# Performance work log

Hardware: AMD Instinct MI355X
Metric: run time of the kernel (lower is better)

The kernel has to match this reference:

```python
import jax, jax.numpy as jnp
import numpy as np

NUM_HEADS = 16
ROPE_BASE = 10000.0

def _rope(x):
    # x: (B, T, H, hd), rotate-half 1D RoPE over temporal axis
    B, T, H, hd = x.shape
    inv_freq = 1.0 / (ROPE_BASE ** (jnp.arange(0, hd, 2, dtype=jnp.float32) / hd))  # (hd/2,)
    freqs = jnp.arange(T, dtype=jnp.float32)[:, None] * inv_freq[None, :]            # (T, hd/2)
    emb = jnp.concatenate([freqs, freqs], axis=-1)                                    # (T, hd)
    cos = jnp.cos(emb)[None, :, None, :]
    sin = jnp.sin(emb)[None, :, None, :]
    x1, x2 = jnp.split(x, 2, axis=-1)
    rot = jnp.concatenate([-x2, x1], axis=-1)
    return x * cos + rot * sin

def setup_inputs() -> dict:
    key = jax.random.key(0)
    ks = jax.random.split(key, 7)
    B, T, S, D = 4, 16, 256, 2048
    std = 0.02
    return {
        'v_p': jax.random.normal(ks[0], (B, T, S, D), jnp.float32),
        'v_f': jax.random.normal(ks[1], (B, T, S, D), jnp.float32),
        'a_p': jax.random.normal(ks[2], (B, T, D), jnp.float32),
        'a_f': jax.random.normal(ks[3], (B, T, D), jnp.float32),
        'W_qkv': jax.random.normal(ks[4], (D, 3 * D), jnp.float32) * std,
        'W_proj': jax.random.normal(ks[5], (D, D), jnp.float32) * std,
        'b_proj': jnp.zeros((D,), jnp.float32),
    }

def reference(v_p, v_f, a_p, a_f, W_qkv, W_proj, b_proj):
    B, T_p, S, D = v_p.shape
    T_f = v_f.shape[1]
    H = NUM_HEADS
    hd = D // H
    scale = hd ** -0.5
    # pool spatial dim and concatenate streams: [v_p, v_f, a_p, a_f]
    tokens = jnp.concatenate([v_p.mean(axis=2), v_f.mean(axis=2), a_p, a_f], axis=1)  # (B, T, D)
    T = tokens.shape[1]
    qkv = tokens @ W_qkv  # qkv_bias=False
    q, k, v = jnp.split(qkv, 3, axis=-1)
    q = q.reshape(B, T, H, hd)
    k = k.reshape(B, T, H, hd)
    v = v.reshape(B, T, H, hd)
    q = _rope(q)
    k = _rope(k)
    scores = jnp.einsum('bqhd,bkhd->bhqk', q, k) * scale
    causal_mask = jnp.triu(jnp.ones((T, T), dtype=bool), k=1)
    scores = jnp.where(causal_mask[None, None], -jnp.inf, scores)
    attn = jax.nn.softmax(scores, axis=-1)
    out = jnp.einsum('bhqk,bkhd->bqhd', attn, v).reshape(B, T, D)
    out = out @ W_proj + b_proj
    v_p_out = jnp.broadcast_to(out[:, :T_p, None, :], (B, T_p, S, D))
    v_f_out = jnp.broadcast_to(out[:, T_p:T_p + T_f, None, :], (B, T_f, S, D))
    a_p_out = out[:, T_p + T_f:T_p + T_f + T_p]
    a_f_out = out[:, T_p + T_f + T_p:]
    return (v_p_out, v_f_out, a_p_out, a_f_out)
```

## Files before the change

kernel.cpp:

```cpp
#include <hip/hip_runtime.h>
#include <hip/hip_bf16.h>
#include <stdint.h>


using bf16x8v = __attribute__((ext_vector_type(8))) __bf16;
using f32x4v  = __attribute__((ext_vector_type(4))) float;

union Pack8 { __bf16 h[8]; uint4 u; };
union Pack4 { __bf16 h[4]; uint2 u; };

__device__ __forceinline__ int swz(int r, int c) {
    return (r << 6) + ((c ^ (r & 7)) << 3);
}
__device__ __forceinline__ int aswz(int r, int c) {
    return (r << 7) + ((c ^ (r & 31)) << 2);
}

__global__ __launch_bounds__(256) void prep_mean_kernel(
    const float* __restrict__ v_p, const float* __restrict__ v_f,
    float* __restrict__ partials,
    const float* __restrict__ W_qkv, const float* __restrict__ W_proj,
    __bf16* __restrict__ Wt_qkv, __bf16* __restrict__ Wt_proj)
{
    __shared__ float Ls[64][68];
    int bid0 = blockIdx.x;
    if (bid0 < 2048) {
        int bid = bid0;
        int which  = bid >> 10;
        int rem    = bid & 1023;
        int row    = rem >> 4;
        int dchunk = (rem >> 3) & 1;
        int schunk = rem & 7;
        int d = (dchunk << 10) + (threadIdx.x << 2);
        const float* src = (which ? v_f : v_p) + ((size_t)row << 19)
                         + ((size_t)(schunk << 5) << 11) + d;
        float4 a = {0.f, 0.f, 0.f, 0.f};
        #pragma unroll 16
        for (int s = 0; s < 32; ++s) {
            float4 x = *reinterpret_cast<const float4*>(src + ((size_t)s << 11));
            a.x += x.x; a.y += x.y; a.z += x.z; a.w += x.w;
        }
        int pr = which * 64 + row;
        *reinterpret_cast<float4*>(&partials[(size_t)((pr << 3) + schunk) * 2048 + d]) = a;
    } else {
        int bid = bid0 - 2048;
        const float* src; __bf16* dst; int N, tile;
        if (bid < 3072) { src = W_qkv;  dst = Wt_qkv;  N = 6144; tile = bid; }
        else            { src = W_proj; dst = Wt_proj; N = 2048; tile = bid - 3072; }
        int tiles_n = N >> 6;
        int tn = tile % tiles_n;
        int tk = tile / tiles_n;
        int t = threadIdx.x;
        int rb = t >> 4;
        int c4 = (t & 15) << 2;
        #pragma unroll
        for (int s = 0; s < 4; ++s) {
            int r = rb + (s << 4);
            float4 v = *reinterpret_cast<const float4*>(
                src + (size_t)(tk * 64 + r) * N + tn * 64 + c4);
            *reinterpret_cast<float4*>(&Ls[r][c4]) = v;
        }
        __syncthreads();
        int c  = t >> 2;
        int r0 = (t & 3) << 4;
        Pack8 p0, p1;
        #pragma unroll
        for (int i = 0; i < 8; ++i) p0.h[i] = (__bf16)Ls[r0 + i][c];
        #pragma unroll
        for (int i = 0; i < 8; ++i) p1.h[i] = (__bf16)Ls[r0 + 8 + i][c];
        __bf16* drow = dst + (size_t)(tn * 64 + c) * 2048 + tk * 64 + r0;
        *reinterpret_cast<uint4*>(drow)     = p0.u;
        *reinterpret_cast<uint4*>(drow + 8) = p1.u;
    }
}

__global__ __launch_bounds__(256) void tokens_finish_kernel(
    const float* __restrict__ partials, const float* __restrict__ a_p,
    const float* __restrict__ a_f, __bf16* __restrict__ tokens_bf)
{
    int bid = blockIdx.x;
    if (bid < 128) {
        int idx = (bid * 256 + threadIdx.x) * 8;
        int r = idx >> 11;
        int d = idx & 2047;
        float s[8];
        #pragma unroll
        for (int i = 0; i < 8; ++i) s[i] = 0.f;
        #pragma unroll
        for (int sc = 0; sc < 8; ++sc) {
            const float* p = partials + (size_t)((r << 3) + sc) * 2048 + d;
            float4 x0 = *reinterpret_cast<const float4*>(p);
            float4 x1 = *reinterpret_cast<const float4*>(p + 4);
            s[0] += x0.x; s[1] += x0.y; s[2] += x0.z; s[3] += x0.w;
            s[4] += x1.x; s[5] += x1.y; s[6] += x1.z; s[7] += x1.w;
        }
        const float inv = 1.f / 256.f;
        int which = r >> 6, rr = r & 63;
        int b = rr >> 4, tt = rr & 15;
        int tokrow = b * 64 + which * 16 + tt;
        Pack8 p;
        #pragma unroll
        for (int i = 0; i < 8; ++i) p.h[i] = (__bf16)(s[i] * inv);
        *reinterpret_cast<uint4*>(&tokens_bf[(size_t)tokrow * 2048 + d]) = p.u;
    } else {
        int g = (bid - 128) * 256 + threadIdx.x;
        int which = g >> 14;
        int j = g & 16383;
        int b = j >> 12;
        int rr = j & 4095;
        int tt = rr >> 8;
        int gq = rr & 255;
        const float* src = (which ? a_f : a_p) + (size_t)(b * 16 + tt) * 2048 + gq * 8;
        float4 x0 = *reinterpret_cast<const float4*>(src);
        float4 x1 = *reinterpret_cast<const float4*>(src + 4);
        Pack8 p;
        p.h[0] = (__bf16)x0.x; p.h[1] = (__bf16)x0.y; p.h[2] = (__bf16)x0.z; p.h[3] = (__bf16)x0.w;
        p.h[4] = (__bf16)x1.x; p.h[5] = (__bf16)x1.y; p.h[6] = (__bf16)x1.z; p.h[7] = (__bf16)x1.w;
        int tokrow = b * 64 + 32 + which * 16 + tt;
        *reinterpret_cast<uint4*>(&tokens_bf[(size_t)tokrow * 2048 + gq * 8]) = p.u;
    }
}

__global__ __launch_bounds__(256) void gemm_bf16_kernel(
    const __bf16* __restrict__ A, const __bf16* __restrict__ Bt,
    float* __restrict__ C, int N)
{
    __shared__ __bf16 As[4096];
    __shared__ __bf16 Bs[4096];
    const int t = threadIdx.x;
    const int m0 = blockIdx.y << 6;
    const int n0 = blockIdx.x << 6;
    const int kz = blockIdx.z;
    const int kbase = kz << 10;
    const int lane = t & 63;
    const int w = t >> 6;
    const int wm = w << 4;
    const int lrow = lane & 15;
    const int lk = lane >> 4;
    const int srl = lane >> 3;
    const int schunk = lane & 7;

    f32x4v acc[4] = {{0.f,0.f,0.f,0.f},{0.f,0.f,0.f,0.f},
                     {0.f,0.f,0.f,0.f},{0.f,0.f,0.f,0.f}};

    int row_c0 = (w << 4) + srl;
    int row_c1 = row_c0 + 8;
    const __bf16* gA0 = A  + (size_t)(m0 + row_c0) * 2048 + kbase + ((schunk ^ (row_c0 & 7)) << 3);
    const __bf16* gA1 = A  + (size_t)(m0 + row_c1) * 2048 + kbase + ((schunk ^ (row_c1 & 7)) << 3);
    const __bf16* gB0 = Bt + (size_t)(n0 + row_c0) * 2048 + kbase + ((schunk ^ (row_c0 & 7)) << 3);
    const __bf16* gB1 = Bt + (size_t)(n0 + row_c1) * 2048 + kbase + ((schunk ^ (row_c1 & 7)) << 3);
    __bf16* lA0 = &As[(w << 4) << 6];
    __bf16* lA1 = &As[((w << 4) + 8) << 6];
    __bf16* lB0 = &Bs[(w << 4) << 6];
    __bf16* lB1 = &Bs[((w << 4) + 8) << 6];

    for (int kt = 0; kt < 16; ++kt) {
        __syncthreads();
        int ko = kt << 6;
        __builtin_amdgcn_global_load_lds(
            (const __attribute__((address_space(1))) void*)(gA0 + ko),
            (__attribute__((address_space(3))) void*)lA0, 16, 0, 0);
        __builtin_amdgcn_global_load_lds(
            (const __attribute__((address_space(1))) void*)(gA1 + ko),
            (__attribute__((address_space(3))) void*)lA1, 16, 0, 0);
        __builtin_amdgcn_global_load_lds(
            (const __attribute__((address_space(1))) void*)(gB0 + ko),
            (__attribute__((address_space(3))) void*)lB0, 16, 0, 0);
        __builtin_amdgcn_global_load_lds(
            (const __attribute__((address_space(1))) void*)(gB1 + ko),
            (__attribute__((address_space(3))) void*)lB1, 16, 0, 0);
        __syncthreads();
        #pragma unroll
        for (int s = 0; s < 2; ++s) {
            int cA = (s << 2) + lk;
            bf16x8v af = *reinterpret_cast<const bf16x8v*>(&As[swz(wm + lrow, cA)]);
            #pragma unroll
            for (int j = 0; j < 4; ++j) {
                bf16x8v bf = *reinterpret_cast<const bf16x8v*>(&Bs[swz((j << 4) + lrow, cA)]);
                acc[j] = __builtin_amdgcn_mfma_f32_16x16x32_bf16(af, bf, acc[j], 0, 0, 0);
            }
        }
    }
    float* Cz = C + (size_t)kz * 256 * N;
    #pragma unroll
    for (int j = 0; j < 4; ++j) {
        int col = n0 + (j << 4) + lrow;
        #pragma unroll
        for (int e = 0; e < 4; ++e) {
            int row = m0 + wm + (lk << 2) + e;
            Cz[(size_t)row * N + col] = acc[j][e];
        }
    }
}

__global__ __launch_bounds__(256) void attn_kernel(
    const float* __restrict__ qkv, __bf16* __restrict__ attn_out)
{
    __shared__ float q_s[16 * 128];
    __shared__ float k_s[64 * 128];
    const size_t PART = (size_t)256 * 6144;
    int bid = blockIdx.x;
    int qt = bid & 3;
    int h  = (bid >> 2) & 15;
    int b  = bid >> 6;
    int tid = threadIdx.x;
    int qr0 = qt << 4;
    int kcap = qr0 + 16;
    const float* base0 = qkv + (size_t)(b * 64) * 6144 + h * 128;
    const float* base1 = base0 + PART;
    const float L2C = 0.20762050593046012f;
    const float scale = 0.0883883476483184405f;

    {
        int tq = tid >> 4;
        int cg = tid & 15;
        int d = cg << 2;
        int grow = qr0 + tq;
        const float* s0 = base0 + (size_t)grow * 6144;
        const float* s1 = base1 + (size_t)grow * 6144;
        float4 q1a = *reinterpret_cast<const float4*>(s0 + d);
        float4 q1b = *reinterpret_cast<const float4*>(s1 + d);
        float4 q2a = *reinterpret_cast<const float4*>(s0 + d + 64);
        float4 q2b = *reinterpret_cast<const float4*>(s1 + d + 64);
        float4 q1 = {q1a.x + q1b.x, q1a.y + q1b.y, q1a.z + q1b.z, q1a.w + q1b.w};
        float4 q2 = {q2a.x + q2b.x, q2a.y + q2b.y, q2a.z + q2b.z, q2a.w + q2b.w};
        float ft = (float)grow;
        float a0 = ft * exp2f(-(float)(d + 0) * L2C);
        float a1 = ft * exp2f(-(float)(d + 1) * L2C);
        float a2 = ft * exp2f(-(float)(d + 2) * L2C);
        float a3 = ft * exp2f(-(float)(d + 3) * L2C);
        float c0 = cosf(a0), s0f = sinf(a0);
        float c1 = cosf(a1), s1f = sinf(a1);
        float c2 = cosf(a2), s2f = sinf(a2);
        float c3 = cosf(a3), s3f = sinf(a3);
        float4 qa, qb;
        qa.x = q1.x * c0 - q2.x * s0f;  qb.x = q2.x * c0 + q1.x * s0f;
        qa.y = q1.y * c1 - q2.y * s1f;  qb.y = q2.y * c1 + q1.y * s1f;
        qa.z = q1.z * c2 - q2.z * s2f;  qb.z = q2.z * c2 + q1.z * s2f;
        qa.w = q1.w * c3 - q2.w * s3f;  qb.w = q2.w * c3 + q1.w * s3f;
        *reinterpret_cast<float4*>(&q_s[aswz(tq, cg)])      = qa;
        *reinterpret_cast<float4*>(&q_s[aswz(tq, cg + 16)]) = qb;
    }
    #pragma unroll
    for (int r = 0; r < 4; ++r) {
        int idx = tid + (r << 8);
        if (idx < (kcap << 4)) {
            int tk = idx >> 4;
            int cg = idx & 15;
            int d = cg << 2;
            const float* s0 = base0 + (size_t)tk * 6144 + 2048;
            const float* s1 = base1 + (size_t)tk * 6144 + 2048;
            float4 k1a = *reinterpret_cast<const float4*>(s0 + d);
            float4 k1b = *reinterpret_cast<const float4*>(s1 + d);
            float4 k2a = *reinterpret_cast<const float4*>(s0 + d + 64);
            float4 k2b = *reinterpret_cast<const float4*>(s1 + d + 64);
            float4 k1 = {k1a.x + k1b.x, k1a.y + k1b.y, k1a.z + k1b.z, k1a.w + k1b.w};
            float4 k2 = {k2a.x + k2b.x, k2a.y + k2b.y, k2a.z + k2b.z, k2a.w + k2b.w};
            float ft = (float)tk;
            float a0 = ft * exp2f(-(float)(d + 0) * L2C);
            float a1 = ft * exp2f(-(float)(d + 1) * L2C);
            float a2 = ft * exp2f(-(float)(d + 2) * L2C);
            float a3 = ft * exp2f(-(float)(d + 3) * L2C);
            float c0 = cosf(a0), s0f = sinf(a0);
            float c1 = cosf(a1), s1f = sinf(a1);
            float c2 = cosf(a2), s2f = sinf(a2);
            float c3 = cosf(a3), s3f = sinf(a3);
            float4 ka, kb;
            ka.x = k1.x * c0 - k2.x * s0f;  kb.x = k2.x * c0 + k1.x * s0f;
            ka.y = k1.y * c1 - k2.y * s1f;  kb.y = k2.y * c1 + k1.y * s1f;
            ka.z = k1.z * c2 - k2.z * s2f;  kb.z = k2.z * c2 + k1.z * s2f;
            ka.w = k1.w * c3 - k2.w * s3f;  kb.w = k2.w * c3 + k1.w * s3f;
            *reinterpret_cast<float4*>(&k_s[aswz(tk, cg)])      = ka;
            *reinterpret_cast<float4*>(&k_s[aswz(tk, cg + 16)]) = kb;
        }
    }
    __syncthreads();
    int qi = tid >> 4;
    int g  = tid & 15;
    int qg = qr0 + qi;
    float pv[4] = {0.f, 0.f, 0.f, 0.f};
    for (int c = 0; c < 32; ++c) {
        float4 a = *reinterpret_cast<const float4*>(&q_s[aswz(qi, c)]);
        #pragma unroll
        for (int j = 0; j < 4; ++j) {
            if ((j << 4) < kcap) {
                int ki = (j << 4) + g;
                float4 bb = *reinterpret_cast<const float4*>(&k_s[aswz(ki, c)]);
                pv[j] += a.x * bb.x + a.y * bb.y + a.z * bb.z + a.w * bb.w;
            }
        }
    }
    float m = -1e30f;
    #pragma unroll
    for (int j = 0; j < 4; ++j) {
        if ((j << 4) < kcap) {
            int ki = (j << 4) + g;
            pv[j] = (ki <= qg) ? pv[j] * scale : -1e30f;
            m = fmaxf(m, pv[j]);
        }
    }
    m = fmaxf(m, __shfl_xor(m, 1));
    m = fmaxf(m, __shfl_xor(m, 2));
    m = fmaxf(m, __shfl_xor(m, 4));
    m = fmaxf(m, __shfl_xor(m, 8));
    float l = 0.f;
    #pragma unroll
    for (int j = 0; j < 4; ++j) {
        if ((j << 4) < kcap) {
            float e = (pv[j] > -1e29f) ? expf(pv[j] - m) : 0.f;
            pv[j] = e;
            l += e;
        }
    }
    l += __shfl_xor(l, 1);
    l += __shfl_xor(l, 2);
    l += __shfl_xor(l, 4);
    l += __shfl_xor(l, 8);
    float inv_l = 1.f / l;
    __syncthreads();
    float* p_s = q_s;
    #pragma unroll
    for (int j = 0; j < 4; ++j) {
        if ((j << 4) < kcap) p_s[qi * 65 + (j << 4) + g] = pv[j] * inv_l;
    }
    float* v_s = k_s;
    #pragma unroll
    for (int r = 0; r < 8; ++r) {
        int idx = tid + (r << 8);
        if (idx < (kcap << 5)) {
            int tv = idx >> 5;
            int c = idx & 31;
            float4 va = *reinterpret_cast<const float4*>(base0 + (size_t)tv * 6144 + 4096 + (c << 2));
            float4 vb = *reinterpret_cast<const float4*>(base1 + (size_t)tv * 6144 + 4096 + (c << 2));
            float4 vs = {va.x + vb.x, va.y + vb.y, va.z + vb.z, va.w + vb.w};
            *reinterpret_cast<float4*>(&v_s[aswz(tv, c)]) = vs;
        }
    }
    __syncthreads();
    float4 acc[2] = {{0.f,0.f,0.f,0.f},{0.f,0.f,0.f,0.f}};
    for (int ki = 0; ki < kcap; ++ki) {
        float p = p_s[qi * 65 + ki];
        #pragma unroll
        for (int u = 0; u < 2; ++u) {
            float4 vv = *reinterpret_cast<const float4*>(&v_s[aswz(ki, (g << 1) + u)]);
            acc[u].x += p * vv.x;
            acc[u].y += p * vv.y;
            acc[u].z += p * vv.z;
            acc[u].w += p * vv.w;
        }
    }
    __bf16* orow = attn_out + (size_t)(b * 64 + qg) * 2048 + h * 128 + (g << 3);
    #pragma unroll
    for (int u = 0; u < 2; ++u) {
        Pack4 p4;
        p4.h[0] = (__bf16)acc[u].x; p4.h[1] = (__bf16)acc[u].y;
        p4.h[2] = (__bf16)acc[u].z; p4.h[3] = (__bf16)acc[u].w;
        *reinterpret_cast<uint2*>(orow + (u << 2)) = p4.u;
    }
}

__global__ __launch_bounds__(256) void outputs_kernel(
    const float* __restrict__ outp, const float* __restrict__ b_proj,
    float* __restrict__ d_out)
{
    const size_t PART = (size_t)256 * 2048;
    int bid = blockIdx.x;
    if (bid < 4096) {
        int which = bid >> 11;
        int rem = bid & 2047;
        int row = rem >> 5;
        int schunk = rem & 31;
        int b = row >> 4;
        int t = row & 15;
        size_t srcoff = (size_t)(b * 64 + (which << 4) + t) * 2048 + threadIdx.x * 8;
        const float* s0 = outp + srcoff;
        const float* s1 = outp + PART + srcoff;
        float4 a0 = *reinterpret_cast<const float4*>(s0);
        float4 a1 = *reinterpret_cast<const float4*>(s0 + 4);
        float4 b0 = *reinterpret_cast<const float4*>(s1);
        float4 b1 = *reinterpret_cast<const float4*>(s1 + 4);
        float4 v0 = *reinterpret_cast<const float4*>(b_proj + threadIdx.x * 8);
        float4 v1 = *reinterpret_cast<const float4*>(b_proj + threadIdx.x * 8 + 4);
        float4 o0 = {a0.x + b0.x + v0.x, a0.y + b0.y + v0.y,
                     a0.z + b0.z + v0.z, a0.w + b0.w + v0.w};
        float4 o1 = {a1.x + b1.x + v1.x, a1.y + b1.y + v1.y,
                     a1.z + b1.z + v1.z, a1.w + b1.w + v1.w};
        size_t base = (size_t)which * 33554432 +
                      ((size_t)row * 256 + (size_t)schunk * 8) * 2048 + threadIdx.x * 8;
        float* dst = d_out + base;
        #pragma unroll
        for (int s = 0; s < 8; ++s) {
            *reinterpret_cast<float4*>(dst + (size_t)s * 2048)     = o0;
            *reinterpret_cast<float4*>(dst + (size_t)s * 2048 + 4) = o1;
        }
    } else {
        int g8 = (bid - 4096) * 256 + threadIdx.x;
        int which = g8 >> 14;
        int j = g8 & 16383;
        int b = j >> 12;
        int rr = j & 4095;
        int tt = rr >> 8;
        int gq = rr & 255;
        size_t srcoff = (size_t)(b * 64 + 32 + (which << 4) + tt) * 2048 + gq * 8;
        const float* s0 = outp + srcoff;
        const float* s1 = outp + PART + srcoff;
        float4 a0 = *reinterpret_cast<const float4*>(s0);
        float4 a1 = *reinterpret_cast<const float4*>(s0 + 4);
        float4 b0 = *reinterpret_cast<const float4*>(s1);
        float4 b1 = *reinterpret_cast<const float4*>(s1 + 4);
        float4 v0 = *reinterpret_cast<const float4*>(b_proj + gq * 8);
        float4 v1 = *reinterpret_cast<const float4*>(b_proj + gq * 8 + 4);
        float4 x0 = {a0.x + b0.x + v0.x, a0.y + b0.y + v0.y,
                     a0.z + b0.z + v0.z, a0.w + b0.w + v0.w};
        float4 x1 = {a1.x + b1.x + v1.x, a1.y + b1.y + v1.y,
                     a1.z + b1.z + v1.z, a1.w + b1.w + v1.w};
        float* dst = d_out + 67108864 + (size_t)which * 131072 +
                     (size_t)(b * 16 + tt) * 2048 + gq * 8;
        *reinterpret_cast<float4*>(dst)     = x0;
        *reinterpret_cast<float4*>(dst + 4) = x1;
    }
}

extern "C" void kernel_launch(void* const* d_in, const int* in_sizes, int n_in,
                              void* d_out, int out_size, void* d_ws, size_t ws_size,
                              hipStream_t stream)
{
    const float* v_p    = (const float*)d_in[0];
    const float* v_f    = (const float*)d_in[1];
    const float* a_p    = (const float*)d_in[2];
    const float* a_f    = (const float*)d_in[3];
    const float* W_qkv  = (const float*)d_in[4];
    const float* W_proj = (const float*)d_in[5];
    const float* b_proj = (const float*)d_in[6];
    float* out_f = (float*)d_out;

    char* ws = (char*)d_ws;
    __bf16* tokens_bf = (__bf16*)(ws);
    __bf16* Wt_qkv    = (__bf16*)(ws + 1048576);
    __bf16* Wt_proj   = (__bf16*)(ws + 26214400);
    float*  qkv       = (float*)(ws + 34603008);
    __bf16* attn_bf   = (__bf16*)(ws + 47185920);
    float*  outp      = (float*)(ws + 48234496);
    float*  partials  = (float*)(ws + 52428800);

    prep_mean_kernel<<<6144, 256, 0, stream>>>(v_p, v_f, partials,
                                               W_qkv, W_proj, Wt_qkv, Wt_proj);
    tokens_finish_kernel<<<256, 256, 0, stream>>>(partials, a_p, a_f, tokens_bf);
    gemm_bf16_kernel<<<dim3(96, 4, 2), 256, 0, stream>>>(tokens_bf, Wt_qkv, qkv, 6144);
    attn_kernel<<<256, 256, 0, stream>>>(qkv, attn_bf);
    gemm_bf16_kernel<<<dim3(32, 4, 2), 256, 0, stream>>>(attn_bf, Wt_proj, outp, 2048);
    outputs_kernel<<<4224, 256, 0, stream>>>(outp, b_proj, out_f);
}
```

Before: 197.4 us.

## Fuse spatial mean and token finish into single prep kernel without partials

Merges the partial-sum mean kernel and the token finish kernel into one launch. Each block now reduces all 256 spatial positions for its row and d-chunk, using four independent accumulators, and writes bf16 tokens directly. This removes the partials buffer round trip and one kernel launch. In exchange, the reduction runs on far fewer blocks with long serial loops, which may limit memory-level parallelism when streaming the large video inputs.

```diff
diff --git a/kernel.cpp b/kernel.cpp
--- a/kernel.cpp
+++ b/kernel.cpp
@@ -16,94 +16,48 @@
     return (r << 7) + ((c ^ (r & 31)) << 2);
 }
 
-__global__ __launch_bounds__(256) void prep_mean_kernel(
+__global__ __launch_bounds__(256) void prep_all_kernel(
     const float* __restrict__ v_p, const float* __restrict__ v_f,
-    float* __restrict__ partials,
+    const float* __restrict__ a_p, const float* __restrict__ a_f,
     const float* __restrict__ W_qkv, const float* __restrict__ W_proj,
+    __bf16* __restrict__ tokens_bf,
     __bf16* __restrict__ Wt_qkv, __bf16* __restrict__ Wt_proj)
 {
     __shared__ float Ls[64][68];
     int bid0 = blockIdx.x;
-    if (bid0 < 2048) {
-        int bid = bid0;
-        int which  = bid >> 10;
-        int rem    = bid & 1023;
-        int row    = rem >> 4;
-        int dchunk = (rem >> 3) & 1;
-        int schunk = rem & 7;
+    if (bid0 < 256) {
+        int which  = bid0 >> 7;
+        int row    = (bid0 >> 1) & 63;
+        int dchunk = bid0 & 1;
         int d = (dchunk << 10) + (threadIdx.x << 2);
-        const float* src = (which ? v_f : v_p) + ((size_t)row << 19)
-                         + ((size_t)(schunk << 5) << 11) + d;
-        float4 a = {0.f, 0.f, 0.f, 0.f};
-        #pragma unroll 16
-        for (int s = 0; s < 32; ++s) {
-            float4 x = *reinterpret_cast<const float4*>(src + ((size_t)s << 11));
-            a.x += x.x; a.y += x.y; a.z += x.z; a.w += x.w;
-        }
-        int pr = which * 64 + row;
-        *reinterpret_cast<float4*>(&partials[(size_t)((pr << 3) + schunk) * 2048 + d]) = a;
-    } else {
-        int bid = bid0 - 2048;
-        const float* src; __bf16* dst; int N, tile;
-        if (bid < 3072) { src = W_qkv;  dst = Wt_qkv;  N = 6144; tile = bid; }
-        else            { src = W_proj; dst = Wt_proj; N = 2048; tile = bid - 3072; }
-        int tiles_n = N >> 6;
-        int tn = tile % tiles_n;
-        int tk = tile / tiles_n;
-        int t = threadIdx.x;
-        int rb = t >> 4;
-        int c4 = (t & 15) << 2;
-        #pragma unroll
-        for (int s = 0; s < 4; ++s) {
-            int r = rb + (s << 4);
-            float4 v = *reinterpret_cast<const float4*>(
-                src + (size_t)(tk * 64 + r) * N + tn * 64 + c4);
-            *reinterpret_cast<float4*>(&Ls[r][c4]) = v;
-        }
-        __syncthreads();
-        int c  = t >> 2;
-        int r0 = (t & 3) << 4;
-        Pack8 p0, p1;
-        #pragma unroll
-        for (int i = 0; i < 8; ++i) p0.h[i] = (__bf16)Ls[r0 + i][c];
-        #pragma unroll
-        for (int i = 0; i < 8; ++i) p1.h[i] = (__bf16)Ls[r0 + 8 + i][c];
-        __bf16* drow = dst + (size_t)(tn * 64 + c) * 2048 + tk * 64 + r0;
-        *reinterpret_cast<uint4*>(drow)     = p0.u;
-        *reinterpret_cast<uint4*>(drow + 8) = p1.u;
-    }
-}
-
-__global__ __launch_bounds__(256) void tokens_finish_kernel(
-    const float* __restrict__ partials, const float* __restrict__ a_p,
-    const float* __restrict__ a_f, __bf16* __restrict__ tokens_bf)
-{
-    int bid = blockIdx.x;
-    if (bid < 128) {
-        int idx = (bid * 256 + threadIdx.x) * 8;
-        int r = idx >> 11;
-        int d = idx & 2047;
-        float s[8];
-        #pragma unroll
-        for (int i = 0; i < 8; ++i) s[i] = 0.f;
-        #pragma unroll
-        for (int sc = 0; sc < 8; ++sc) {
-            const float* p = partials + (size_t)((r << 3) + sc) * 2048 + d;
-            float4 x0 = *reinterpret_cast<const float4*>(p);
-            float4 x1 = *reinterpret_cast<const float4*>(p + 4);
-            s[0] += x0.x; s[1] += x0.y; s[2] += x0.z; s[3] += x0.w;
-            s[4] += x1.x; s[5] += x1.y; s[6] += x1.z; s[7] += x1.w;
+        const float* src = (which ? v_f : v_p) + ((size_t)row << 19) + d;
+        float4 a0 = {0.f,0.f,0.f,0.f}, a1 = {0.f,0.f,0.f,0.f};
+        float4 a2 = {0.f,0.f,0.f,0.f}, a3 = {0.f,0.f,0.f,0.f};
+        #pragma unroll 4
+        for (int s = 0; s < 256; s += 4) {
+            float4 x0 = *reinterpret_cast<const float4*>(src + ((size_t)(s+0) << 11));
+            float4 x1 = *reinterpret_cast<const float4*>(src + ((size_t)(s+1) << 11));
+            float4 x2 = *reinterpret_cast<const float4*>(src + ((size_t)(s+2) << 11));
+            float4 x3 = *reinterpret_cast<const float4*>(src + ((size_t)(s+3) << 11));
+            a0.x += x0.x; a0.y += x0.y; a0.z += x0.z; a0.w += x0.w;
+            a1.x += x1.x; a1.y += x1.y; a1.z += x1.z; a1.w += x1.w;
+            a2.x += x2.x; a2.y += x2.y; a2.z += x2.z; a2.w += x2.w;
+            a3.x += x3.x; a3.y += x3.y; a3.z += x3.z; a3.w += x3.w;
         }
         const float inv = 1.f / 256.f;
-        int which = r >> 6, rr = r & 63;
-        int b = rr >> 4, tt = rr & 15;
+        float4 o;
+        o.x = (a0.x + a1.x + a2.x + a3.x) * inv;
+        o.y = (a0.y + a1.y + a2.y + a3.y) * inv;
+        o.z = (a0.z + a1.z + a2.z + a3.z) * inv;
+        o.w = (a0.w + a1.w + a2.w + a3.w) * inv;
+        int b = row >> 4, tt = row & 15;
         int tokrow = b * 64 + which * 16 + tt;
-        Pack8 p;
-        #pragma unroll
-        for (int i = 0; i < 8; ++i) p.h[i] = (__bf16)(s[i] * inv);
-        *reinterpret_cast<uint4*>(&tokens_bf[(size_t)tokrow * 2048 + d]) = p.u;
-    } else {
-        int g = (bid - 128) * 256 + threadIdx.x;
+        Pack4 p4;
+        p4.h[0] = (__bf16)o.x; p4.h[1] = (__bf16)o.y;
+        p4.h[2] = (__bf16)o.z; p4.h[3] = (__bf16)o.w;
+        *reinterpret_cast<uint2*>(&tokens_bf[(size_t)tokrow * 2048 + d]) = p4.u;
+    } else if (bid0 < 384) {
+        int g = (bid0 - 256) * 256 + threadIdx.x;
         int which = g >> 14;
         int j = g & 16383;
         int b = j >> 12;
@@ -118,6 +72,35 @@
         p.h[4] = (__bf16)x1.x; p.h[5] = (__bf16)x1.y; p.h[6] = (__bf16)x1.z; p.h[7] = (__bf16)x1.w;
         int tokrow = b * 64 + 32 + which * 16 + tt;
         *reinterpret_cast<uint4*>(&tokens_bf[(size_t)tokrow * 2048 + gq * 8]) = p.u;
+    } else {
+        int bid = bid0 - 384;
+        const float* src; __bf16* dst; int N, tile;
+        if (bid < 3072) { src = W_qkv;  dst = Wt_qkv;  N = 6144; tile = bid; }
+        else            { src = W_proj; dst = Wt_proj; N = 2048; tile = bid - 3072; }
+        int tiles_n = N >> 6;
+        int tn = tile % tiles_n;
+        int tk = tile / tiles_n;
+        int t = threadIdx.x;
+        int rb = t >> 4;
+        int c4 = (t & 15) << 2;
+        #pragma unroll
+        for (int s = 0; s < 4; ++s) {
+            int r = rb + (s << 4);
+            float4 v = *reinterpret_cast<const float4*>(
+                src + (size_t)(tk * 64 + r) * N + tn * 64 + c4);
+            *reinterpret_cast<float4*>(&Ls[r][c4]) = v;
+        }
+        __syncthreads();
+        int c  = t >> 2;
+        int r0 = (t & 3) << 4;
+        Pack8 p0, p1;
+        #pragma unroll
+        for (int i = 0; i < 8; ++i) p0.h[i] = (__bf16)Ls[r0 + i][c];
+        #pragma unroll
+        for (int i = 0; i < 8; ++i) p1.h[i] = (__bf16)Ls[r0 + 8 + i][c];
+        __bf16* drow = dst + (size_t)(tn * 64 + c) * 2048 + tk * 64 + r0;
+        *reinterpret_cast<uint4*>(drow)     = p0.u;
+        *reinterpret_cast<uint4*>(drow + 8) = p1.u;
     }
 }
 
@@ -441,11 +424,10 @@
     float*  qkv       = (float*)(ws + 34603008);
     __bf16* attn_bf   = (__bf16*)(ws + 47185920);
     float*  outp      = (float*)(ws + 48234496);
-    float*  partials  = (float*)(ws + 52428800);
-
-    prep_mean_kernel<<<6144, 256, 0, stream>>>(v_p, v_f, partials,
-                                               W_qkv, W_proj, Wt_qkv, Wt_proj);
-    tokens_finish_kernel<<<256, 256, 0, stream>>>(partials, a_p, a_f, tokens_bf);
+
+    prep_all_kernel<<<4480, 256, 0, stream>>>(v_p, v_f, a_p, a_f,
+                                              W_qkv, W_proj,
+                                              tokens_bf, Wt_qkv, Wt_proj);
     gemm_bf16_kernel<<<dim3(96, 4, 2), 256, 0, stream>>>(tokens_bf, Wt_qkv, qkv, 6144);
     attn_kernel<<<256, 256, 0, stream>>>(qkv, attn_bf);
     gemm_bf16_kernel<<<dim3(32, 4, 2), 256, 0, stream>>>(attn_bf, Wt_proj, outp, 2048);
```

Measured after the change: 197.2 us. About the same (-0.1%).
